# Kernel optimization log

Hardware: AMD Instinct MI355X
Metric: run time of the kernel (lower is better)

Reference implementation:

```python
import jax, jax.numpy as jnp
import numpy as np

C = 128       # in_channels
B = 256       # number of graph pairs (inter.shape[0])
N1_PER = 32   # nodes per graph, side 1
N2_PER = 32   # nodes per graph, side 2


def prelu(x, s):
    return jnp.where(x >= 0, x, s * x)


def _lin(k, fan_in, fan_out):
    return jax.random.normal(k, (fan_in, fan_out), jnp.float32) / np.sqrt(fan_in)


def setup_inputs() -> dict:
    key = jax.random.key(0)
    ks = jax.random.split(key, 16)
    N1, N2 = B * N1_PER, B * N2_PER
    d1 = np.full(B, N1_PER, np.int64)
    d2 = np.full(B, N2_PER, np.int64)
    batch_1 = np.repeat(np.arange(B), d1)
    batch_2 = np.repeat(np.arange(B), d2)
    # node offsets per graph (exclusive cumsum)
    s1 = np.concatenate([[0], np.cumsum(d1)[:-1]])
    s2 = np.concatenate([[0], np.cumsum(d2)[:-1]])
    # ragged pairwise cross-product indices, same as the torch loop
    ind_1 = np.concatenate([np.repeat(np.arange(d1[g]), d2[g]) + s1[g] for g in range(B)])
    ind_2 = np.concatenate([np.tile(np.arange(d2[g]), d1[g]) + s1[g] * 0 + s2[g] for g in range(B)])
    batch_ans = np.repeat(np.arange(B), d1 * d2)

    inp = {
        "x_1": jax.random.normal(ks[0], (N1, C), jnp.float32),
        "x_2": jax.random.normal(ks[1], (N2, C), jnp.float32),
        "inter": jax.random.normal(ks[2], (B, C), jnp.float32),
        "batch_1": jnp.asarray(batch_1, jnp.int32),
        "batch_2": jnp.asarray(batch_2, jnp.int32),
        "ind_1": jnp.asarray(ind_1, jnp.int32),
        "ind_2": jnp.asarray(ind_2, jnp.int32),
        "batch_ans": jnp.asarray(batch_ans, jnp.int32),
        # glorot-style param 'a'
        "a": jax.random.normal(ks[3], (C,), jnp.float32) * np.sqrt(2.0 / (1 + C)),
        # mlp: PReLU, Linear(2C,2C), PReLU, Linear(2C,C), PReLU, Linear(C,C)
        "Wm1": _lin(ks[4], 2 * C, 2 * C), "bm1": jnp.zeros((2 * C,), jnp.float32),
        "Wm2": _lin(ks[5], 2 * C, C),     "bm2": jnp.zeros((C,), jnp.float32),
        "Wm3": _lin(ks[6], C, C),         "bm3": jnp.zeros((C,), jnp.float32),
        "pm0": jnp.float32(0.25), "pm1": jnp.float32(0.25), "pm2": jnp.float32(0.25),
        # weight_1: Linear(2C,C), PReLU, Linear(C,1), Sigmoid
        "Wg1a": _lin(ks[7], 2 * C, C), "bg1a": jnp.zeros((C,), jnp.float32),
        "Wg1b": _lin(ks[8], C, 1),     "bg1b": jnp.zeros((1,), jnp.float32),
        "pw1": jnp.float32(0.25),
        # weight_2: Linear(2C,C), PReLU, Linear(C,1), Sigmoid
        "Wg2a": _lin(ks[9], 2 * C, C), "bg2a": jnp.zeros((C,), jnp.float32),
        "Wg2b": _lin(ks[10], C, 1),    "bg2b": jnp.zeros((1,), jnp.float32),
        "pw2": jnp.float32(0.25),
    }
    return inp


def reference(x_1, x_2, inter, batch_1, batch_2, ind_1, ind_2, batch_ans,
              a, Wm1, bm1, Wm2, bm2, Wm3, bm3, pm0, pm1, pm2,
              Wg1a, bg1a, Wg1b, bg1b, pw1, Wg2a, bg2a, Wg2b, bg2b, pw2):
    Bn = inter.shape[0]
    # global_add_pool readouts, broadcast back per node (repeat_interleave == gather by batch id)
    r1 = jax.ops.segment_sum(x_1, batch_1, num_segments=Bn)          # [B, C]
    r2 = jax.ops.segment_sum(x_2, batch_2, num_segments=Bn)          # [B, C]
    x1s = jnp.concatenate([x_1, r2[batch_1]], axis=1)                # [N1, 2C]
    x2s = jnp.concatenate([x_2, r1[batch_2]], axis=1)                # [N2, 2C]
    # gating MLPs -> sigmoid scalar per node
    w1 = jax.nn.sigmoid(prelu(x1s @ Wg1a + bg1a, pw1) @ Wg1b + bg1b)  # [N1, 1]
    w2 = jax.nn.sigmoid(prelu(x2s @ Wg2a + bg2a, pw2) @ Wg2b + bg2b)  # [N2, 1]
    x1g = x_1 * w1
    x2g = x_2 * w2
    # ragged pairwise gather
    xi = x1g[ind_1]                                                  # [P, C]
    xj = x2g[ind_2]                                                  # [P, C]
    h = jnp.concatenate([xi, xj], axis=1)                            # [P, 2C]
    h = prelu(h, pm0) @ Wm1 + bm1
    h = prelu(h, pm1) @ Wm2 + bm2
    h = prelu(h, pm2) @ Wm3 + bm3                                    # [P, C]
    ssi = (a * h) * inter[batch_ans]                                 # [P, C]
    logit = jax.ops.segment_sum(jnp.sum(ssi, axis=-1), batch_ans, num_segments=Bn)  # [B]
    return (logit, xi, xj)
```

## Files before the change

kernel.cpp:

```cpp
#include <hip/hip_runtime.h>
#include <hip/hip_bf16.h>
#include <hip/hip_fp16.h>

typedef __attribute__((ext_vector_type(8))) _Float16 half8;
typedef __attribute__((ext_vector_type(2))) _Float16 f16x2;
typedef __attribute__((ext_vector_type(8))) short short8;
typedef __attribute__((ext_vector_type(4))) float f32x4;

#define C_ 128

__device__ __forceinline__ unsigned short f2h(float f) {
    return __builtin_bit_cast(unsigned short, (_Float16)f);
}
__device__ __forceinline__ f16x2 pkrtz(float x, float y) {
    return __builtin_bit_cast(f16x2, __builtin_amdgcn_cvt_pkrtz(x, y));
}
__device__ __forceinline__ float prelu_f(float x, float s) {
    return fmaxf(x, 0.f) + s * fminf(x, 0.f);
}
__device__ __forceinline__ half8 prelu_h8(half8 x, half8 sl) {
    half8 z = {0, 0, 0, 0, 0, 0, 0, 0};
    half8 mx = __builtin_elementwise_max(x, z);
    half8 mn = __builtin_elementwise_min(x, z);
    return mn * sl + mx;
}

__global__ __launch_bounds__(256) void prep_weights(
    const float* __restrict__ Wm1, const float* __restrict__ Wm2,
    const float* __restrict__ Wg1a, const float* __restrict__ Wg2a,
    short* __restrict__ ws)
{
    int id = blockIdx.x * 256 + threadIdx.x;
    if (id < 8192) {
        int c = id >> 5, kb = (id & 31) * 8;
        short8 v;
        #pragma unroll
        for (int e = 0; e < 8; ++e) v[e] = (short)f2h(Wm1[(kb + e) * 256 + c]);
        *(short8*)(ws + c * 256 + kb) = v;
    }
    if (id < 4096) {
        int c = id >> 5, kb = (id & 31) * 8;
        short8 a, b, d;
        #pragma unroll
        for (int e = 0; e < 8; ++e) {
            a[e] = (short)f2h(Wm2 [(kb + e) * C_ + c]);
            b[e] = (short)f2h(Wg1a[(kb + e) * C_ + c]);
            d[e] = (short)f2h(Wg2a[(kb + e) * C_ + c]);
        }
        *(short8*)(ws + 65536  + c * 256 + kb) = a;
        *(short8*)(ws + 98304  + c * 256 + kb) = b;
        *(short8*)(ws + 131072 + c * 256 + kb) = d;
    }
}

__global__ __launch_bounds__(512, 1) void interactions_fused(
    const float* __restrict__ x1_, const float* __restrict__ x2_,
    const float* __restrict__ inter, const float* __restrict__ aP,
    const short* __restrict__ Wt,
    const float* __restrict__ bm1, const float* __restrict__ bm2,
    const float* __restrict__ Wm3, const float* __restrict__ bm3,
    const float* __restrict__ pm0p, const float* __restrict__ pm1p,
    const float* __restrict__ pm2p,
    const float* __restrict__ bg1a, const float* __restrict__ Wg1b,
    const float* __restrict__ bg1b, const float* __restrict__ pw1p,
    const float* __restrict__ bg2a, const float* __restrict__ Wg2b,
    const float* __restrict__ bg2b, const float* __restrict__ pw2p,
    float* __restrict__ out)
{
    __shared__ __align__(16) float xs1[32 * 132];
    __shared__ __align__(16) float xs2[32 * 132];
    __shared__ __align__(16) unsigned char Ub[16384];
    __shared__ __align__(16) unsigned char Vb[16384];
    __shared__ __align__(16) float rr[2][C_];
    __shared__ __align__(16) float tv[C_];
    __shared__ __align__(16) float ugs[C_];
    __shared__ float wgtp[2][2][32];
    __shared__ float red[4];
    __shared__ float cbias_s;
    __shared__ int cnt1, cnt2;

    const int t = threadIdx.x;
    const int g = blockIdx.x;
    const int lane = t & 63;
    const int w = t >> 6;

    if (t == 0) { cnt1 = 0; cnt2 = 0; }

    {
        const float* s1 = x1_ + (size_t)g * 4096;
        const float* s2 = x2_ + (size_t)g * 4096;
        #pragma unroll
        for (int q = 0; q < 2; ++q) {
            int idx = q * 512 + t;
            int row = idx >> 5, cc = (idx & 31) * 4;
            f32x4 v1 = *(const f32x4*)(s1 + idx * 4);
            f32x4 v2 = *(const f32x4*)(s2 + idx * 4);
            *(f32x4*)(xs1 + row * 132 + cc) = v1;
            *(f32x4*)(xs2 + row * 132 + cc) = v2;
        }
    }
    __syncthreads();

    if (t < 128) {
        float s = 0.f;
        for (int n = 0; n < 32; ++n) s += xs1[n * 132 + t];
        rr[0][t] = s;
    } else if (t < 256) {
        int c = t - 128;
        float s = 0.f;
        for (int n = 0; n < 32; ++n) s += xs2[n * 132 + c];
        rr[1][c] = s;
    } else if (t < 384) {
        int c = t - 256;
        tv[c] = aP[c] * inter[(size_t)g * C_ + c];
    }
    __syncthreads();

    {
        const int task = w & 3;
        const int half = w >> 2;
        const int sd = task >> 1;
        const int rt = task & 1;
        const float* xs = sd ? xs2 : xs1;
        const float* roth = sd ? rr[0] : rr[1];
        const short* WgT = Wt + (sd ? 131072 : 98304);
        const float* bga = sd ? bg2a : bg1a;
        const float* wgb = sd ? Wg2b : Wg1b;
        const float pw  = sd ? pw2p[0] : pw1p[0];
        const int row = rt * 16 + (lane & 15);
        const int kg = (lane >> 4) * 8;

        half8 afr[8];
        #pragma unroll
        for (int kt = 0; kt < 8; ++kt) {
            const float* p = (kt < 4) ? (xs + row * 132 + kt * 32 + kg)
                                      : (roth + (kt - 4) * 32 + kg);
            f32x4 lo = *(const f32x4*)p;
            f32x4 hi = *(const f32x4*)(p + 4);
            f16x2 a = pkrtz(lo[0], lo[1]);
            f16x2 b = pkrtz(lo[2], lo[3]);
            f16x2 c = pkrtz(hi[0], hi[1]);
            f16x2 d = pkrtz(hi[2], hi[3]);
            half8 fr = {a[0], a[1], b[0], b[1], c[0], c[1], d[0], d[1]};
            afr[kt] = fr;
        }
        float pr[4] = {0, 0, 0, 0};
        #pragma unroll
        for (int cq = 0; cq < 4; ++cq) {
            const int ct = half * 4 + cq;
            const int c = ct * 16 + (lane & 15);
            const short* wp = WgT + c * 256 + kg;
            f32x4 acc = {0, 0, 0, 0};
            #pragma unroll
            for (int kt = 0; kt < 8; ++kt)
                acc = __builtin_amdgcn_mfma_f32_16x16x32_f16(
                          afr[kt], *(const half8*)(wp + kt * 32), acc, 0, 0, 0);
            const float bgac = bga[c], wgbc = wgb[c];
            #pragma unroll
            for (int r = 0; r < 4; ++r)
                pr[r] += prelu_f(acc[r] + bgac, pw) * wgbc;
        }
        #pragma unroll
        for (int r = 0; r < 4; ++r) {
            float p = pr[r];
            p += __shfl_xor(p, 1); p += __shfl_xor(p, 2);
            p += __shfl_xor(p, 4); p += __shfl_xor(p, 8);
            if ((lane & 15) == 0)
                wgtp[half][sd][rt * 16 + (lane >> 4) * 4 + r] = p;
        }
    }
    __syncthreads();

    {
        const float bgb1 = bg1b[0], bgb2 = bg2b[0];
        const int cc = (t & 31) * 4;
        const int tn = t >> 5;
        #pragma unroll
        for (int m = 0; m < 2; ++m) {
            const int nr = m * 16 + tn;
            const float w1v = 1.f / (1.f + __expf(-(wgtp[0][0][nr] + wgtp[1][0][nr] + bgb1)));
            const float w2v = 1.f / (1.f + __expf(-(wgtp[0][1][nr] + wgtp[1][1][nr] + bgb2)));
            f32x4 v1 = *(f32x4*)(xs1 + nr * 132 + cc);
            f32x4 v2 = *(f32x4*)(xs2 + nr * 132 + cc);
            v1 *= w1v; v2 *= w2v;
            *(f32x4*)(xs1 + nr * 132 + cc) = v1;
            *(f32x4*)(xs2 + nr * 132 + cc) = v2;
        }
    }
    __syncthreads();

    if (w >= 4) {
        if (t < 384) {
            const int c = t - 256;
            const float* wr = Wm3 + c * C_;
            float s0 = 0, s1 = 0, s2 = 0, s3 = 0;
            #pragma unroll
            for (int k = 0; k < 128; k += 4) {
                f32x4 wv = *(const f32x4*)(wr + k);
                s0 += wv[0] * tv[k];     s1 += wv[1] * tv[k + 1];
                s2 += wv[2] * tv[k + 2]; s3 += wv[3] * tv[k + 3];
            }
            ugs[c] = (s0 + s1) + (s2 + s3);
        } else if (w == 7) {
            float p = bm3[lane] * tv[lane] + bm3[64 + lane] * tv[64 + lane];
            #pragma unroll
            for (int m = 1; m < 64; m <<= 1) p += __shfl_xor(p, m);
            if (lane == 0) cbias_s = p;
        }
        __threadfence_block();
        if (lane == 0)
            __hip_atomic_fetch_add(&cnt1, 1, __ATOMIC_RELEASE, __HIP_MEMORY_SCOPE_WORKGROUP);

        const int ws_ = w - 4;
        float* oxi = out + 256 + (size_t)g * 131072;
        float* oxj = out + 256 + 33554432 + (size_t)g * 131072;
        const int ccl = (lane & 31) * 4;

        #pragma unroll
        for (int blk = 0; blk < 8; ++blk) {
            const int i = ws_ * 8 + blk;
            f32x4 v = *(const f32x4*)(xs1 + i * 132 + ccl);
            float* base = oxi + i * 4096 + lane * 4;
            #pragma unroll
            for (int s2 = 0; s2 < 16; ++s2)
                __builtin_nontemporal_store(v, (f32x4*)(base + s2 * 256));
        }
        f32x4 vj[16];
        #pragma unroll
        for (int s2 = 0; s2 < 16; ++s2) {
            const int jn = (2 * s2 + (lane >> 5)) & 31;
            vj[s2] = *(const f32x4*)(xs2 + jn * 132 + ccl);
        }
        #pragma unroll
        for (int so = 0; so < 8; ++so) {
            float* bb = oxj + (size_t)(ws_ * 256 + so * 32) * 128 + lane * 4;
            #pragma unroll
            for (int s2 = 0; s2 < 16; ++s2)
                __builtin_nontemporal_store(vj[s2], (f32x4*)(bb + s2 * 256));
        }
    } else {
        {
            const int sd = w >> 1;
            const int rt = w & 1;
            const float* xs = sd ? xs2 : xs1;
            const float pm0 = pm0p[0];
            const int row = rt * 16 + (lane & 15);
            const int kg = (lane >> 4) * 8;
            half8 afr[4];
            #pragma unroll
            for (int kt = 0; kt < 4; ++kt) {
                const float* p = xs + row * 132 + kt * 32 + kg;
                f32x4 lo = *(const f32x4*)p;
                f32x4 hi = *(const f32x4*)(p + 4);
                f16x2 a = pkrtz(prelu_f(lo[0], pm0), prelu_f(lo[1], pm0));
                f16x2 b = pkrtz(prelu_f(lo[2], pm0), prelu_f(lo[3], pm0));
                f16x2 c = pkrtz(prelu_f(hi[0], pm0), prelu_f(hi[1], pm0));
                f16x2 d = pkrtz(prelu_f(hi[2], pm0), prelu_f(hi[3], pm0));
                half8 fr = {a[0], a[1], b[0], b[1], c[0], c[1], d[0], d[1]};
                afr[kt] = fr;
            }
            unsigned char* dst = sd ? Vb : Ub;
            #pragma unroll
            for (int ct = 0; ct < 16; ++ct) {
                const int c = ct * 16 + (lane & 15);
                const short* wp = Wt + c * 256 + sd * 128 + kg;
                f32x4 av = {0, 0, 0, 0};
                #pragma unroll
                for (int kt = 0; kt < 4; ++kt)
                    av = __builtin_amdgcn_mfma_f32_16x16x32_f16(
                             afr[kt], *(const half8*)(wp + kt * 32), av, 0, 0, 0);
                const float badd = sd ? 0.f : bm1[c];
                #pragma unroll
                for (int r = 0; r < 4; ++r) {
                    const int n = rt * 16 + (lane >> 4) * 4 + r;
                    const int off = n * 512 + ((2 * c + ((n & 7) << 6)) & 511);
                    *(unsigned short*)(dst + off) = f2h(av[r] + badd);
                }
            }
        }
        __threadfence_block();
        if (lane == 0)
            __hip_atomic_fetch_add(&cnt1, 1, __ATOMIC_RELEASE, __HIP_MEMORY_SCOPE_WORKGROUP);
        while (__hip_atomic_load(&cnt1, __ATOMIC_ACQUIRE, __HIP_MEMORY_SCOPE_WORKGROUP) < 8)
            __builtin_amdgcn_s_sleep(1);
        __threadfence_block();

        float psum = 0.f;
        {
            const float pm1v = pm1p[0], pm2v = pm2p[0];
            const _Float16 pm1s = (_Float16)pm1v;
            const half8 pm1h = {pm1s, pm1s, pm1s, pm1s, pm1s, pm1s, pm1s, pm1s};
            const int cl = lane & 15;
            const int kg8 = (lane >> 4) * 8;
            const int kg16 = kg8 * 2;
            const int c0 = (2 * w) * 16 + cl, c1 = (2 * w + 1) * 16 + cl;
            half8 Bf0[8], Bf1[8];
            const short* w2p0 = Wt + 65536 + c0 * 256 + kg8;
            const short* w2p1 = Wt + 65536 + c1 * 256 + kg8;
            #pragma unroll
            for (int kt = 0; kt < 8; ++kt) {
                Bf0[kt] = *(const half8*)(w2p0 + kt * 32);
                Bf1[kt] = *(const half8*)(w2p1 + kt * 32);
            }
            const float bm2c0 = bm2[c0], bm2c1 = bm2[c1];
            const float ug0 = ugs[c0], ug1 = ugs[c1];

            half8 VrA[8], VrB[8];
            {
                const int j0 = cl, j1 = 16 + cl;
                #pragma unroll
                for (int kt = 0; kt < 8; ++kt) {
                    const int koff = kt * 64 + kg16;
                    VrA[kt] = *(const half8*)(Vb + j0 * 512 + ((koff + ((j0 & 7) << 6)) & 511));
                    VrB[kt] = *(const half8*)(Vb + j1 * 512 + ((koff + ((j1 & 7) << 6)) & 511));
                }
            }

            #pragma unroll 2
            for (int i = 0; i < 32; ++i) {
                const int ub = i * 512, us = (i & 7) << 6;
                half8 u8[8];
                #pragma unroll
                for (int kt = 0; kt < 8; ++kt)
                    u8[kt] = *(const half8*)(Ub + ub + ((kt * 64 + kg16 + us) & 511));
                f32x4 acc0 = {0, 0, 0, 0}, acc1 = {0, 0, 0, 0};
                f32x4 acc2 = {0, 0, 0, 0}, acc3 = {0, 0, 0, 0};
                #pragma unroll
                for (int kt = 0; kt < 8; ++kt) {
                    half8 afA = prelu_h8(u8[kt] + VrA[kt], pm1h);
                    half8 afB = prelu_h8(u8[kt] + VrB[kt], pm1h);
                    acc0 = __builtin_amdgcn_mfma_f32_16x16x32_f16(afA, Bf0[kt], acc0, 0, 0, 0);
                    acc1 = __builtin_amdgcn_mfma_f32_16x16x32_f16(afA, Bf1[kt], acc1, 0, 0, 0);
                    acc2 = __builtin_amdgcn_mfma_f32_16x16x32_f16(afB, Bf0[kt], acc2, 0, 0, 0);
                    acc3 = __builtin_amdgcn_mfma_f32_16x16x32_f16(afB, Bf1[kt], acc3, 0, 0, 0);
                }
                #pragma unroll
                for (int r = 0; r < 4; ++r) {
                    psum += prelu_f(acc0[r] + bm2c0, pm2v) * ug0;
                    psum += prelu_f(acc1[r] + bm2c1, pm2v) * ug1;
                    psum += prelu_f(acc2[r] + bm2c0, pm2v) * ug0;
                    psum += prelu_f(acc3[r] + bm2c1, pm2v) * ug1;
                }
            }
        }
        #pragma unroll
        for (int m = 1; m < 64; m <<= 1) psum += __shfl_xor(psum, m);
        if (lane == 0) {
            red[w] = psum;
            __threadfence_block();
            __hip_atomic_fetch_add(&cnt2, 1, __ATOMIC_RELEASE, __HIP_MEMORY_SCOPE_WORKGROUP);
            if (w == 0) {
                while (__hip_atomic_load(&cnt2, __ATOMIC_ACQUIRE, __HIP_MEMORY_SCOPE_WORKGROUP) < 4)
                    __builtin_amdgcn_s_sleep(1);
                __threadfence_block();
                out[g] = red[0] + red[1] + red[2] + red[3] + 1024.f * cbias_s;
            }
        }
    }
}

extern "C" void kernel_launch(void* const* d_in, const int* in_sizes, int n_in,
                              void* d_out, int out_size, void* d_ws, size_t ws_size,
                              hipStream_t stream) {
    const float* x1   = (const float*)d_in[0];
    const float* x2   = (const float*)d_in[1];
    const float* itr  = (const float*)d_in[2];
    const float* a    = (const float*)d_in[8];
    const float* Wm1  = (const float*)d_in[9];
    const float* bm1  = (const float*)d_in[10];
    const float* Wm2  = (const float*)d_in[11];
    const float* bm2  = (const float*)d_in[12];
    const float* Wm3  = (const float*)d_in[13];
    const float* bm3  = (const float*)d_in[14];
    const float* pm0  = (const float*)d_in[15];
    const float* pm1  = (const float*)d_in[16];
    const float* pm2  = (const float*)d_in[17];
    const float* Wg1a = (const float*)d_in[18];
    const float* bg1a = (const float*)d_in[19];
    const float* Wg1b = (const float*)d_in[20];
    const float* bg1b = (const float*)d_in[21];
    const float* pw1  = (const float*)d_in[22];
    const float* Wg2a = (const float*)d_in[23];
    const float* bg2a = (const float*)d_in[24];
    const float* Wg2b = (const float*)d_in[25];
    const float* bg2b = (const float*)d_in[26];
    const float* pw2  = (const float*)d_in[27];
    float* out = (float*)d_out;
    short* Wt = (short*)d_ws;

    hipLaunchKernelGGL(prep_weights, dim3(32), dim3(256), 0, stream,
                       Wm1, Wm2, Wg1a, Wg2a, Wt);
    hipLaunchKernelGGL(interactions_fused, dim3(256), dim3(512), 0, stream,
                       x1, x2, itr, a, Wt, bm1, bm2, Wm3, bm3,
                       pm0, pm1, pm2, bg1a, Wg1b, bg1b, pw1,
                       bg2a, Wg2b, bg2b, pw2, out);
}
```

Before: 86.34 us.

## Distribute xi/xj output writes across all waves via shared work counter

```diff
diff --git a/kernel.cpp b/kernel.cpp
--- a/kernel.cpp
+++ b/kernel.cpp
@@ -77,14 +77,14 @@
     __shared__ float wgtp[2][2][32];
     __shared__ float red[4];
     __shared__ float cbias_s;
-    __shared__ int cnt1, cnt2;
+    __shared__ int cnt1, cnt2, ucnt;
 
     const int t = threadIdx.x;
     const int g = blockIdx.x;
     const int lane = t & 63;
     const int w = t >> 6;
 
-    if (t == 0) { cnt1 = 0; cnt2 = 0; }
+    if (t == 0) { cnt1 = 0; cnt2 = 0; ucnt = 0; }
 
     {
         const float* s1 = x1_ + (size_t)g * 4096;
@@ -210,34 +210,6 @@
         __threadfence_block();
         if (lane == 0)
             __hip_atomic_fetch_add(&cnt1, 1, __ATOMIC_RELEASE, __HIP_MEMORY_SCOPE_WORKGROUP);
-
-        const int ws_ = w - 4;
-        float* oxi = out + 256 + (size_t)g * 131072;
-        float* oxj = out + 256 + 33554432 + (size_t)g * 131072;
-        const int ccl = (lane & 31) * 4;
-
-        #pragma unroll
-        for (int blk = 0; blk < 8; ++blk) {
-            const int i = ws_ * 8 + blk;
-            f32x4 v = *(const f32x4*)(xs1 + i * 132 + ccl);
-            float* base = oxi + i * 4096 + lane * 4;
-            #pragma unroll
-            for (int s2 = 0; s2 < 16; ++s2)
-                __builtin_nontemporal_store(v, (f32x4*)(base + s2 * 256));
-        }
-        f32x4 vj[16];
-        #pragma unroll
-        for (int s2 = 0; s2 < 16; ++s2) {
-            const int jn = (2 * s2 + (lane >> 5)) & 31;
-            vj[s2] = *(const f32x4*)(xs2 + jn * 132 + ccl);
-        }
-        #pragma unroll
-        for (int so = 0; so < 8; ++so) {
-            float* bb = oxj + (size_t)(ws_ * 256 + so * 32) * 128 + lane * 4;
-            #pragma unroll
-            for (int s2 = 0; s2 < 16; ++s2)
-                __builtin_nontemporal_store(vj[s2], (f32x4*)(bb + s2 * 256));
-        }
     } else {
         {
             const int sd = w >> 1;
@@ -354,6 +326,40 @@
                     __builtin_amdgcn_s_sleep(1);
                 __threadfence_block();
                 out[g] = red[0] + red[1] + red[2] + red[3] + 1024.f * cbias_s;
+            }
+        }
+    }
+
+    {
+        float* oxi = out + 256 + (size_t)g * 131072;
+        float* oxj = out + 256 + 33554432 + (size_t)g * 131072;
+        const int ccl = (lane & 31) * 4;
+
+        f32x4 vj[16];
+        #pragma unroll
+        for (int s2 = 0; s2 < 16; ++s2) {
+            const int jn = 2 * s2 + (lane >> 5);
+            vj[s2] = *(const f32x4*)(xs2 + jn * 132 + ccl);
+        }
+
+        for (;;) {
+            int u = 0;
+            if (lane == 0)
+                u = __hip_atomic_fetch_add(&ucnt, 1, __ATOMIC_RELAXED,
+                                           __HIP_MEMORY_SCOPE_WORKGROUP);
+            u = __shfl(u, 0);
+            if (u >= 64) break;
+            if (u < 32) {
+                f32x4 v = *(const f32x4*)(xs1 + u * 132 + ccl);
+                float* base = oxi + u * 4096 + lane * 4;
+                #pragma unroll
+                for (int s2 = 0; s2 < 16; ++s2)
+                    *(f32x4*)(base + s2 * 256) = v;
+            } else {
+                float* bb = oxj + (size_t)(u - 32) * 4096 + lane * 4;
+                #pragma unroll
+                for (int s2 = 0; s2 < 16; ++s2)
+                    *(f32x4*)(bb + s2 * 256) = vj[s2];
             }
         }
     }
```

Result: faster. 83.70 us (-3.0%).

## Split fused kernel into compute stage and wide expand/logit kernel

Applied to the files above, without the earlier changes.

```diff
diff --git a/kernel.cpp b/kernel.cpp
--- a/kernel.cpp
+++ b/kernel.cpp
@@ -8,6 +8,7 @@
 typedef __attribute__((ext_vector_type(4))) float f32x4;
 
 #define C_ 128
+#define XJ_OFF 33554432
 
 __device__ __forceinline__ unsigned short f2h(float f) {
     return __builtin_bit_cast(unsigned short, (_Float16)f);
@@ -53,50 +54,37 @@
     }
 }
 
-__global__ __launch_bounds__(512, 1) void interactions_fused(
+__global__ __launch_bounds__(256, 2) void compute_stage(
     const float* __restrict__ x1_, const float* __restrict__ x2_,
     const float* __restrict__ inter, const float* __restrict__ aP,
     const short* __restrict__ Wt,
-    const float* __restrict__ bm1, const float* __restrict__ bm2,
     const float* __restrict__ Wm3, const float* __restrict__ bm3,
-    const float* __restrict__ pm0p, const float* __restrict__ pm1p,
-    const float* __restrict__ pm2p,
     const float* __restrict__ bg1a, const float* __restrict__ Wg1b,
     const float* __restrict__ bg1b, const float* __restrict__ pw1p,
     const float* __restrict__ bg2a, const float* __restrict__ Wg2b,
     const float* __restrict__ bg2b, const float* __restrict__ pw2p,
-    float* __restrict__ out)
+    float* __restrict__ wsF, float* __restrict__ out)
 {
     __shared__ __align__(16) float xs1[32 * 132];
     __shared__ __align__(16) float xs2[32 * 132];
-    __shared__ __align__(16) unsigned char Ub[16384];
-    __shared__ __align__(16) unsigned char Vb[16384];
     __shared__ __align__(16) float rr[2][C_];
     __shared__ __align__(16) float tv[C_];
-    __shared__ __align__(16) float ugs[C_];
-    __shared__ float wgtp[2][2][32];
-    __shared__ float red[4];
-    __shared__ float cbias_s;
-    __shared__ int cnt1, cnt2;
+    __shared__ float wgt[2][32];
 
     const int t = threadIdx.x;
     const int g = blockIdx.x;
     const int lane = t & 63;
     const int w = t >> 6;
 
-    if (t == 0) { cnt1 = 0; cnt2 = 0; }
-
     {
         const float* s1 = x1_ + (size_t)g * 4096;
         const float* s2 = x2_ + (size_t)g * 4096;
         #pragma unroll
-        for (int q = 0; q < 2; ++q) {
-            int idx = q * 512 + t;
+        for (int q = 0; q < 4; ++q) {
+            int idx = q * 256 + t;
             int row = idx >> 5, cc = (idx & 31) * 4;
-            f32x4 v1 = *(const f32x4*)(s1 + idx * 4);
-            f32x4 v2 = *(const f32x4*)(s2 + idx * 4);
-            *(f32x4*)(xs1 + row * 132 + cc) = v1;
-            *(f32x4*)(xs2 + row * 132 + cc) = v2;
+            *(f32x4*)(xs1 + row * 132 + cc) = *(const f32x4*)(s1 + idx * 4);
+            *(f32x4*)(xs2 + row * 132 + cc) = *(const f32x4*)(s2 + idx * 4);
         }
     }
     __syncthreads();
@@ -105,27 +93,24 @@
         float s = 0.f;
         for (int n = 0; n < 32; ++n) s += xs1[n * 132 + t];
         rr[0][t] = s;
-    } else if (t < 256) {
+        tv[t] = aP[t] * inter[(size_t)g * C_ + t];
+    } else {
         int c = t - 128;
         float s = 0.f;
         for (int n = 0; n < 32; ++n) s += xs2[n * 132 + c];
         rr[1][c] = s;
-    } else if (t < 384) {
-        int c = t - 256;
-        tv[c] = aP[c] * inter[(size_t)g * C_ + c];
-    }
-    __syncthreads();
-
-    {
-        const int task = w & 3;
-        const int half = w >> 2;
-        const int sd = task >> 1;
-        const int rt = task & 1;
+    }
+    __syncthreads();
+
+    {
+        const int sd = w >> 1;
+        const int rt = w & 1;
         const float* xs = sd ? xs2 : xs1;
         const float* roth = sd ? rr[0] : rr[1];
         const short* WgT = Wt + (sd ? 131072 : 98304);
         const float* bga = sd ? bg2a : bg1a;
         const float* wgb = sd ? Wg2b : Wg1b;
+        const float bgb = sd ? bg2b[0] : bg1b[0];
         const float pw  = sd ? pw2p[0] : pw1p[0];
         const int row = rt * 16 + (lane & 15);
         const int kg = (lane >> 4) * 8;
@@ -146,8 +131,7 @@
         }
         float pr[4] = {0, 0, 0, 0};
         #pragma unroll
-        for (int cq = 0; cq < 4; ++cq) {
-            const int ct = half * 4 + cq;
+        for (int ct = 0; ct < 8; ++ct) {
             const int c = ct * 16 + (lane & 15);
             const short* wp = WgT + c * 256 + kg;
             f32x4 acc = {0, 0, 0, 0};
@@ -166,20 +150,19 @@
             p += __shfl_xor(p, 1); p += __shfl_xor(p, 2);
             p += __shfl_xor(p, 4); p += __shfl_xor(p, 8);
             if ((lane & 15) == 0)
-                wgtp[half][sd][rt * 16 + (lane >> 4) * 4 + r] = p;
-        }
-    }
-    __syncthreads();
-
-    {
-        const float bgb1 = bg1b[0], bgb2 = bg2b[0];
+                wgt[sd][rt * 16 + (lane >> 4) * 4 + r] =
+                    1.f / (1.f + __expf(-(p + bgb)));
+        }
+    }
+    __syncthreads();
+
+    {
         const int cc = (t & 31) * 4;
         const int tn = t >> 5;
         #pragma unroll
-        for (int m = 0; m < 2; ++m) {
-            const int nr = m * 16 + tn;
-            const float w1v = 1.f / (1.f + __expf(-(wgtp[0][0][nr] + wgtp[1][0][nr] + bgb1)));
-            const float w2v = 1.f / (1.f + __expf(-(wgtp[0][1][nr] + wgtp[1][1][nr] + bgb2)));
+        for (int m = 0; m < 4; ++m) {
+            const int nr = m * 8 + tn;
+            const float w1v = wgt[0][nr], w2v = wgt[1][nr];
             f32x4 v1 = *(f32x4*)(xs1 + nr * 132 + cc);
             f32x4 v2 = *(f32x4*)(xs2 + nr * 132 + cc);
             v1 *= w1v; v2 *= w2v;
@@ -189,10 +172,20 @@
     }
     __syncthreads();
 
-    if (w >= 4) {
-        if (t < 384) {
-            const int c = t - 256;
-            const float* wr = Wm3 + c * C_;
+    {
+        float* oxi = out + 256 + (size_t)g * 131072;
+        float* oxj = oxi + XJ_OFF;
+        #pragma unroll
+        for (int m = 0; m < 4; ++m) {
+            const int row = m * 8 + (t >> 5);
+            const int c4 = (t & 31) * 4;
+            *(f32x4*)(oxi + row * 4096 + c4) = *(const f32x4*)(xs1 + row * 132 + c4);
+            const int idx4 = m * 256 + t;
+            const int j = idx4 >> 5;
+            *(f32x4*)(oxj + idx4 * 4) = *(const f32x4*)(xs2 + j * 132 + (idx4 & 31) * 4);
+        }
+        if (t < 128) {
+            const float* wr = Wm3 + t * C_;
             float s0 = 0, s1 = 0, s2 = 0, s3 = 0;
             #pragma unroll
             for (int k = 0; k < 128; k += 4) {
@@ -200,163 +193,180 @@
                 s0 += wv[0] * tv[k];     s1 += wv[1] * tv[k + 1];
                 s2 += wv[2] * tv[k + 2]; s3 += wv[3] * tv[k + 3];
             }
-            ugs[c] = (s0 + s1) + (s2 + s3);
-        } else if (w == 7) {
+            wsF[g * 132 + t] = (s0 + s1) + (s2 + s3);
+        } else if (t < 192) {
             float p = bm3[lane] * tv[lane] + bm3[64 + lane] * tv[64 + lane];
             #pragma unroll
             for (int m = 1; m < 64; m <<= 1) p += __shfl_xor(p, m);
-            if (lane == 0) cbias_s = p;
-        }
-        __threadfence_block();
-        if (lane == 0)
-            __hip_atomic_fetch_add(&cnt1, 1, __ATOMIC_RELEASE, __HIP_MEMORY_SCOPE_WORKGROUP);
-
-        const int ws_ = w - 4;
-        float* oxi = out + 256 + (size_t)g * 131072;
-        float* oxj = out + 256 + 33554432 + (size_t)g * 131072;
-        const int ccl = (lane & 31) * 4;
-
-        #pragma unroll
-        for (int blk = 0; blk < 8; ++blk) {
-            const int i = ws_ * 8 + blk;
-            f32x4 v = *(const f32x4*)(xs1 + i * 132 + ccl);
-            float* base = oxi + i * 4096 + lane * 4;
-            #pragma unroll
-            for (int s2 = 0; s2 < 16; ++s2)
-                __builtin_nontemporal_store(v, (f32x4*)(base + s2 * 256));
-        }
-        f32x4 vj[16];
-        #pragma unroll
-        for (int s2 = 0; s2 < 16; ++s2) {
-            const int jn = (2 * s2 + (lane >> 5)) & 31;
-            vj[s2] = *(const f32x4*)(xs2 + jn * 132 + ccl);
-        }
-        #pragma unroll
-        for (int so = 0; so < 8; ++so) {
-            float* bb = oxj + (size_t)(ws_ * 256 + so * 32) * 128 + lane * 4;
-            #pragma unroll
-            for (int s2 = 0; s2 < 16; ++s2)
-                __builtin_nontemporal_store(vj[s2], (f32x4*)(bb + s2 * 256));
-        }
-    } else {
+            if (lane == 0) wsF[g * 132 + 128] = p;
+        }
+    }
+}
+
+__global__ __launch_bounds__(256) void expand_logit(
+    const short* __restrict__ Wt, const float* __restrict__ wsF,
+    const float* __restrict__ bm1, const float* __restrict__ bm2,
+    const float* __restrict__ pm0p, const float* __restrict__ pm1p,
+    const float* __restrict__ pm2p, float* __restrict__ out)
+{
+    const int b = blockIdx.x;
+    const int t = threadIdx.x;
+
+    if (b >= 256) {
+        const int sb = b - 256;
+        for (int u = sb; u < 16384; u += 1792) {
+            const int g = u >> 6, r = u & 63;
+            float* oxi = out + 256 + (size_t)g * 131072;
+            if (r < 32) {
+                const f32x4 v = *(const f32x4*)(oxi + r * 4096 + (t & 31) * 4);
+                float* base = oxi + r * 4096;
+                #pragma unroll
+                for (int s = 0; s < 4; ++s)
+                    *(f32x4*)(base + (s * 256 + t) * 4) = v;
+            } else {
+                float* oxj = oxi + XJ_OFF;
+                const int i = r - 32;
+                #pragma unroll
+                for (int s = 0; s < 4; ++s) {
+                    const int idx4 = s * 256 + t;
+                    f32x4 v = *(const f32x4*)(oxj + idx4 * 4);
+                    *(f32x4*)(oxj + i * 4096 + idx4 * 4) = v;
+                }
+            }
+        }
+        return;
+    }
+
+    __shared__ __align__(16) float xs1[32 * 132];
+    __shared__ __align__(16) float xs2[32 * 132];
+    __shared__ __align__(16) unsigned char Ub[16384];
+    __shared__ __align__(16) unsigned char Vb[16384];
+    __shared__ __align__(16) float ugs[C_];
+    __shared__ float red[4];
+
+    const int g = b;
+    const int lane = t & 63;
+    const int w = t >> 6;
+    const float* oxi = out + 256 + (size_t)g * 131072;
+    const float* oxj = oxi + XJ_OFF;
+
+    #pragma unroll
+    for (int m = 0; m < 4; ++m) {
+        const int row = m * 8 + (t >> 5);
+        const int c4 = (t & 31) * 4;
+        *(f32x4*)(xs1 + row * 132 + c4) = *(const f32x4*)(oxi + row * 4096 + c4);
+        const int idx4 = m * 256 + t;
+        const int j = idx4 >> 5;
+        *(f32x4*)(xs2 + j * 132 + (idx4 & 31) * 4) = *(const f32x4*)(oxj + idx4 * 4);
+    }
+    if (t < 128) ugs[t] = wsF[g * 132 + t];
+    __syncthreads();
+
+    {
+        const int sd = w >> 1;
+        const int rt = w & 1;
+        const float* xs = sd ? xs2 : xs1;
+        const float pm0 = pm0p[0];
+        const int row = rt * 16 + (lane & 15);
+        const int kg = (lane >> 4) * 8;
+        half8 afr[4];
+        #pragma unroll
+        for (int kt = 0; kt < 4; ++kt) {
+            const float* p = xs + row * 132 + kt * 32 + kg;
+            f32x4 lo = *(const f32x4*)p;
+            f32x4 hi = *(const f32x4*)(p + 4);
+            f16x2 a = pkrtz(prelu_f(lo[0], pm0), prelu_f(lo[1], pm0));
+            f16x2 b = pkrtz(prelu_f(lo[2], pm0), prelu_f(lo[3], pm0));
+            f16x2 c = pkrtz(prelu_f(hi[0], pm0), prelu_f(hi[1], pm0));
+            f16x2 d = pkrtz(prelu_f(hi[2], pm0), prelu_f(hi[3], pm0));
+            half8 fr = {a[0], a[1], b[0], b[1], c[0], c[1], d[0], d[1]};
+            afr[kt] = fr;
+        }
+        unsigned char* dst = sd ? Vb : Ub;
+        #pragma unroll
+        for (int ct = 0; ct < 16; ++ct) {
+            const int c = ct * 16 + (lane & 15);
+            const short* wp = Wt + c * 256 + sd * 128 + kg;
+            f32x4 av = {0, 0, 0, 0};
+            #pragma unroll
+            for (int kt = 0; kt < 4; ++kt)
+                av = __builtin_amdgcn_mfma_f32_16x16x32_f16(
+                         afr[kt], *(const half8*)(wp + kt * 32), av, 0, 0, 0);
+            const float badd = sd ? 0.f : bm1[c];
+            #pragma unroll
+            for (int r = 0; r < 4; ++r) {
+                const int n = rt * 16 + (lane >> 4) * 4 + r;
+                const int off = n * 512 + ((2 * c + ((n & 7) << 6)) & 511);
+                *(unsigned short*)(dst + off) = f2h(av[r] + badd);
+            }
+        }
+    }
+    __syncthreads();
+
+    float psum = 0.f;
+    {
+        const float pm1v = pm1p[0], pm2v = pm2p[0];
+        const _Float16 pm1s = (_Float16)pm1v;
+        const half8 pm1h = {pm1s, pm1s, pm1s, pm1s, pm1s, pm1s, pm1s, pm1s};
+        const int cl = lane & 15;
+        const int kg8 = (lane >> 4) * 8;
+        const int kg16 = kg8 * 2;
+        const int c0 = (2 * w) * 16 + cl, c1 = (2 * w + 1) * 16 + cl;
+        half8 Bf0[8], Bf1[8];
+        const short* w2p0 = Wt + 65536 + c0 * 256 + kg8;
+        const short* w2p1 = Wt + 65536 + c1 * 256 + kg8;
+        #pragma unroll
+        for (int kt = 0; kt < 8; ++kt) {
+            Bf0[kt] = *(const half8*)(w2p0 + kt * 32);
+            Bf1[kt] = *(const half8*)(w2p1 + kt * 32);
+        }
+        const float bm2c0 = bm2[c0], bm2c1 = bm2[c1];
+        const float ug0 = ugs[c0], ug1 = ugs[c1];
+
+        half8 VrA[8], VrB[8];
         {
-            const int sd = w >> 1;
-            const int rt = w & 1;
-            const float* xs = sd ? xs2 : xs1;
-            const float pm0 = pm0p[0];
-            const int row = rt * 16 + (lane & 15);
-            const int kg = (lane >> 4) * 8;
-            half8 afr[4];
-            #pragma unroll
-            for (int kt = 0; kt < 4; ++kt) {
-                const float* p = xs + row * 132 + kt * 32 + kg;
-                f32x4 lo = *(const f32x4*)p;
-                f32x4 hi = *(const f32x4*)(p + 4);
-                f16x2 a = pkrtz(prelu_f(lo[0], pm0), prelu_f(lo[1], pm0));
-                f16x2 b = pkrtz(prelu_f(lo[2], pm0), prelu_f(lo[3], pm0));
-                f16x2 c = pkrtz(prelu_f(hi[0], pm0), prelu_f(hi[1], pm0));
-                f16x2 d = pkrtz(prelu_f(hi[2], pm0), prelu_f(hi[3], pm0));
-                half8 fr = {a[0], a[1], b[0], b[1], c[0], c[1], d[0], d[1]};
-                afr[kt] = fr;
-            }
-            unsigned char* dst = sd ? Vb : Ub;
-            #pragma unroll
-            for (int ct = 0; ct < 16; ++ct) {
-                const int c = ct * 16 + (lane & 15);
-                const short* wp = Wt + c * 256 + sd * 128 + kg;
-                f32x4 av = {0, 0, 0, 0};
-                #pragma unroll
-                for (int kt = 0; kt < 4; ++kt)
-                    av = __builtin_amdgcn_mfma_f32_16x16x32_f16(
-                             afr[kt], *(const half8*)(wp + kt * 32), av, 0, 0, 0);
-                const float badd = sd ? 0.f : bm1[c];
-                #pragma unroll
-                for (int r = 0; r < 4; ++r) {
-                    const int n = rt * 16 + (lane >> 4) * 4 + r;
-                    const int off = n * 512 + ((2 * c + ((n & 7) << 6)) & 511);
-                    *(unsigned short*)(dst + off) = f2h(av[r] + badd);
-                }
-            }
-        }
-        __threadfence_block();
-        if (lane == 0)
-            __hip_atomic_fetch_add(&cnt1, 1, __ATOMIC_RELEASE, __HIP_MEMORY_SCOPE_WORKGROUP);
-        while (__hip_atomic_load(&cnt1, __ATOMIC_ACQUIRE, __HIP_MEMORY_SCOPE_WORKGROUP) < 8)
-            __builtin_amdgcn_s_sleep(1);
-        __threadfence_block();
-
-        float psum = 0.f;
-        {
-            const float pm1v = pm1p[0], pm2v = pm2p[0];
-            const _Float16 pm1s = (_Float16)pm1v;
-            const half8 pm1h = {pm1s, pm1s, pm1s, pm1s, pm1s, pm1s, pm1s, pm1s};
-            const int cl = lane & 15;
-            const int kg8 = (lane >> 4) * 8;
-            const int kg16 = kg8 * 2;
-            const int c0 = (2 * w) * 16 + cl, c1 = (2 * w + 1) * 16 + cl;
-            half8 Bf0[8], Bf1[8];
-            const short* w2p0 = Wt + 65536 + c0 * 256 + kg8;
-            const short* w2p1 = Wt + 65536 + c1 * 256 + kg8;
+            const int j0 = cl, j1 = 16 + cl;
             #pragma unroll
             for (int kt = 0; kt < 8; ++kt) {
-                Bf0[kt] = *(const half8*)(w2p0 + kt * 32);
-                Bf1[kt] = *(const half8*)(w2p1 + kt * 32);
-            }
-            const float bm2c0 = bm2[c0], bm2c1 = bm2[c1];
-            const float ug0 = ugs[c0], ug1 = ugs[c1];
-
-            half8 VrA[8], VrB[8];
-            {
-                const int j0 = cl, j1 = 16 + cl;
-                #pragma unroll
-                for (int kt = 0; kt < 8; ++kt) {
-                    const int koff = kt * 64 + kg16;
-                    VrA[kt] = *(const half8*)(Vb + j0 * 512 + ((koff + ((j0 & 7) << 6)) & 511));
-                    VrB[kt] = *(const half8*)(Vb + j1 * 512 + ((koff + ((j1 & 7) << 6)) & 511));
-                }
-            }
-
-            #pragma unroll 2
-            for (int i = 0; i < 32; ++i) {
-                const int ub = i * 512, us = (i & 7) << 6;
-                half8 u8[8];
-                #pragma unroll
-                for (int kt = 0; kt < 8; ++kt)
-                    u8[kt] = *(const half8*)(Ub + ub + ((kt * 64 + kg16 + us) & 511));
-                f32x4 acc0 = {0, 0, 0, 0}, acc1 = {0, 0, 0, 0};
-                f32x4 acc2 = {0, 0, 0, 0}, acc3 = {0, 0, 0, 0};
-                #pragma unroll
-                for (int kt = 0; kt < 8; ++kt) {
-                    half8 afA = prelu_h8(u8[kt] + VrA[kt], pm1h);
-                    half8 afB = prelu_h8(u8[kt] + VrB[kt], pm1h);
-                    acc0 = __builtin_amdgcn_mfma_f32_16x16x32_f16(afA, Bf0[kt], acc0, 0, 0, 0);
-                    acc1 = __builtin_amdgcn_mfma_f32_16x16x32_f16(afA, Bf1[kt], acc1, 0, 0, 0);
-                    acc2 = __builtin_amdgcn_mfma_f32_16x16x32_f16(afB, Bf0[kt], acc2, 0, 0, 0);
-                    acc3 = __builtin_amdgcn_mfma_f32_16x16x32_f16(afB, Bf1[kt], acc3, 0, 0, 0);
-                }
-                #pragma unroll
-                for (int r = 0; r < 4; ++r) {
-                    psum += prelu_f(acc0[r] + bm2c0, pm2v) * ug0;
-                    psum += prelu_f(acc1[r] + bm2c1, pm2v) * ug1;
-                    psum += prelu_f(acc2[r] + bm2c0, pm2v) * ug0;
-                    psum += prelu_f(acc3[r] + bm2c1, pm2v) * ug1;
-                }
-            }
-        }
-        #pragma unroll
-        for (int m = 1; m < 64; m <<= 1) psum += __shfl_xor(psum, m);
-        if (lane == 0) {
-            red[w] = psum;
-            __threadfence_block();
-            __hip_atomic_fetch_add(&cnt2, 1, __ATOMIC_RELEASE, __HIP_MEMORY_SCOPE_WORKGROUP);
-            if (w == 0) {
-                while (__hip_atomic_load(&cnt2, __ATOMIC_ACQUIRE, __HIP_MEMORY_SCOPE_WORKGROUP) < 4)
-                    __builtin_amdgcn_s_sleep(1);
-                __threadfence_block();
-                out[g] = red[0] + red[1] + red[2] + red[3] + 1024.f * cbias_s;
-            }
-        }
-    }
+                const int koff = kt * 64 + kg16;
+                VrA[kt] = *(const half8*)(Vb + j0 * 512 + ((koff + ((j0 & 7) << 6)) & 511));
+                VrB[kt] = *(const half8*)(Vb + j1 * 512 + ((koff + ((j1 & 7) << 6)) & 511));
+            }
+        }
+
+        #pragma unroll 2
+        for (int i = 0; i < 32; ++i) {
+            const int ub = i * 512, us = (i & 7) << 6;
+            half8 u8[8];
+            #pragma unroll
+            for (int kt = 0; kt < 8; ++kt)
+                u8[kt] = *(const half8*)(Ub + ub + ((kt * 64 + kg16 + us) & 511));
+            f32x4 acc0 = {0, 0, 0, 0}, acc1 = {0, 0, 0, 0};
+            f32x4 acc2 = {0, 0, 0, 0}, acc3 = {0, 0, 0, 0};
+            #pragma unroll
+            for (int kt = 0; kt < 8; ++kt) {
+                half8 afA = prelu_h8(u8[kt] + VrA[kt], pm1h);
+                half8 afB = prelu_h8(u8[kt] + VrB[kt], pm1h);
+                acc0 = __builtin_amdgcn_mfma_f32_16x16x32_f16(afA, Bf0[kt], acc0, 0, 0, 0);
+                acc1 = __builtin_amdgcn_mfma_f32_16x16x32_f16(afA, Bf1[kt], acc1, 0, 0, 0);
+                acc2 = __builtin_amdgcn_mfma_f32_16x16x32_f16(afB, Bf0[kt], acc2, 0, 0, 0);
+                acc3 = __builtin_amdgcn_mfma_f32_16x16x32_f16(afB, Bf1[kt], acc3, 0, 0, 0);
+            }
+            #pragma unroll
+            for (int r = 0; r < 4; ++r) {
+                psum += prelu_f(acc0[r] + bm2c0, pm2v) * ug0;
+                psum += prelu_f(acc1[r] + bm2c1, pm2v) * ug1;
+                psum += prelu_f(acc2[r] + bm2c0, pm2v) * ug0;
+                psum += prelu_f(acc3[r] + bm2c1, pm2v) * ug1;
+            }
+        }
+    }
+    #pragma unroll
+    for (int m = 1; m < 64; m <<= 1) psum += __shfl_xor(psum, m);
+    if (lane == 0) red[w] = psum;
+    __syncthreads();
+    if (t == 0)
+        out[g] = red[0] + red[1] + red[2] + red[3] + 1024.f * wsF[g * 132 + 128];
 }
 
 extern "C" void kernel_launch(void* const* d_in, const int* in_sizes, int n_in,
@@ -387,11 +397,14 @@
     const float* pw2  = (const float*)d_in[27];
     float* out = (float*)d_out;
     short* Wt = (short*)d_ws;
+    float* wsF = (float*)(Wt + 163840);
 
     hipLaunchKernelGGL(prep_weights, dim3(32), dim3(256), 0, stream,
                        Wm1, Wm2, Wg1a, Wg2a, Wt);
-    hipLaunchKernelGGL(interactions_fused, dim3(256), dim3(512), 0, stream,
-                       x1, x2, itr, a, Wt, bm1, bm2, Wm3, bm3,
-                       pm0, pm1, pm2, bg1a, Wg1b, bg1b, pw1,
-                       bg2a, Wg2b, bg2b, pw2, out);
-}
+    hipLaunchKernelGGL(compute_stage, dim3(256), dim3(256), 0, stream,
+                       x1, x2, itr, a, Wt, Wm3, bm3,
+                       bg1a, Wg1b, bg1b, pw1, bg2a, Wg2b, bg2b, pw2,
+                       wsF, out);
+    hipLaunchKernelGGL(expand_logit, dim3(2048), dim3(256), 0, stream,
+                       Wt, wsF, bm1, bm2, pm0, pm1, pm2, out);
+}
```

Result: slower. 93.98 us (+8.9%).

## Split xi/xj output broadcast into a separate wide expansion kernel

Applied to the files above, without the earlier changes.

```diff
diff --git a/kernel.cpp b/kernel.cpp
--- a/kernel.cpp
+++ b/kernel.cpp
@@ -8,6 +8,7 @@
 typedef __attribute__((ext_vector_type(4))) float f32x4;
 
 #define C_ 128
+#define XJ_OFF 33554432
 
 __device__ __forceinline__ unsigned short f2h(float f) {
     return __builtin_bit_cast(unsigned short, (_Float16)f);
@@ -53,7 +54,7 @@
     }
 }
 
-__global__ __launch_bounds__(512, 1) void interactions_fused(
+__global__ __launch_bounds__(512, 1) void interactions_core(
     const float* __restrict__ x1_, const float* __restrict__ x2_,
     const float* __restrict__ inter, const float* __restrict__ aP,
     const short* __restrict__ Wt,
@@ -93,10 +94,8 @@
         for (int q = 0; q < 2; ++q) {
             int idx = q * 512 + t;
             int row = idx >> 5, cc = (idx & 31) * 4;
-            f32x4 v1 = *(const f32x4*)(s1 + idx * 4);
-            f32x4 v2 = *(const f32x4*)(s2 + idx * 4);
-            *(f32x4*)(xs1 + row * 132 + cc) = v1;
-            *(f32x4*)(xs2 + row * 132 + cc) = v2;
+            *(f32x4*)(xs1 + row * 132 + cc) = *(const f32x4*)(s1 + idx * 4);
+            *(f32x4*)(xs2 + row * 132 + cc) = *(const f32x4*)(s2 + idx * 4);
         }
     }
     __syncthreads();
@@ -189,6 +188,9 @@
     }
     __syncthreads();
 
+    float* oxi = out + 256 + (size_t)g * 131072;
+    float* oxj = oxi + XJ_OFF;
+
     if (w >= 4) {
         if (t < 384) {
             const int c = t - 256;
@@ -211,32 +213,24 @@
         if (lane == 0)
             __hip_atomic_fetch_add(&cnt1, 1, __ATOMIC_RELEASE, __HIP_MEMORY_SCOPE_WORKGROUP);
 
-        const int ws_ = w - 4;
-        float* oxi = out + 256 + (size_t)g * 131072;
-        float* oxj = out + 256 + 33554432 + (size_t)g * 131072;
-        const int ccl = (lane & 31) * 4;
-
-        #pragma unroll
-        for (int blk = 0; blk < 8; ++blk) {
-            const int i = ws_ * 8 + blk;
-            f32x4 v = *(const f32x4*)(xs1 + i * 132 + ccl);
-            float* base = oxi + i * 4096 + lane * 4;
-            #pragma unroll
-            for (int s2 = 0; s2 < 16; ++s2)
-                __builtin_nontemporal_store(v, (f32x4*)(base + s2 * 256));
-        }
-        f32x4 vj[16];
-        #pragma unroll
-        for (int s2 = 0; s2 < 16; ++s2) {
-            const int jn = (2 * s2 + (lane >> 5)) & 31;
-            vj[s2] = *(const f32x4*)(xs2 + jn * 132 + ccl);
-        }
-        #pragma unroll
-        for (int so = 0; so < 8; ++so) {
-            float* bb = oxj + (size_t)(ws_ * 256 + so * 32) * 128 + lane * 4;
-            #pragma unroll
-            for (int s2 = 0; s2 < 16; ++s2)
-                __builtin_nontemporal_store(vj[s2], (f32x4*)(bb + s2 * 256));
+        if (w < 6) {
+            const int base = (w - 4) * 512;
+            #pragma unroll
+            for (int m = 0; m < 8; ++m) {
+                const int idx = base + m * 64 + lane;
+                const int row = idx >> 5, c4 = (idx & 31) * 4;
+                *(f32x4*)(oxi + (size_t)row * 4096 + c4) =
+                    *(const f32x4*)(xs1 + row * 132 + c4);
+            }
+        } else {
+            const int base = (w - 6) * 512;
+            #pragma unroll
+            for (int m = 0; m < 8; ++m) {
+                const int idx = base + m * 64 + lane;
+                const int row = idx >> 5, c4 = (idx & 31) * 4;
+                *(f32x4*)(oxj + idx * 4) =
+                    *(const f32x4*)(xs2 + row * 132 + c4);
+            }
         }
     } else {
         {
@@ -355,6 +349,40 @@
                 __threadfence_block();
                 out[g] = red[0] + red[1] + red[2] + red[3] + 1024.f * cbias_s;
             }
+        }
+    }
+}
+
+__global__ __launch_bounds__(256) void expand_out(float* __restrict__ out)
+{
+    const int b = blockIdx.x;
+    const int t = threadIdx.x;
+
+    if (b < 256) {
+        float* oxi = out + 256 + (size_t)b * 131072;
+        const int c4 = (t & 31) * 4;
+        f32x4 v[32];
+        #pragma unroll
+        for (int i = 0; i < 32; ++i)
+            v[i] = *(const f32x4*)(oxi + (size_t)i * 4096 + c4);
+        #pragma unroll
+        for (int i = 0; i < 32; ++i) {
+            float* base = oxi + (size_t)i * 4096;
+            #pragma unroll
+            for (int s = 0; s < 4; ++s)
+                *(f32x4*)(base + (s * 256 + t) * 4) = v[i];
+        }
+    } else {
+        float* oxj = out + 256 + XJ_OFF + (size_t)(b - 256) * 131072;
+        f32x4 vj[4];
+        #pragma unroll
+        for (int s = 0; s < 4; ++s)
+            vj[s] = *(const f32x4*)(oxj + (s * 256 + t) * 4);
+        for (int i = 1; i < 32; ++i) {
+            float* base = oxj + (size_t)i * 4096;
+            #pragma unroll
+            for (int s = 0; s < 4; ++s)
+                *(f32x4*)(base + (s * 256 + t) * 4) = vj[s];
         }
     }
 }
@@ -390,8 +418,9 @@
 
     hipLaunchKernelGGL(prep_weights, dim3(32), dim3(256), 0, stream,
                        Wm1, Wm2, Wg1a, Wg2a, Wt);
-    hipLaunchKernelGGL(interactions_fused, dim3(256), dim3(512), 0, stream,
+    hipLaunchKernelGGL(interactions_core, dim3(256), dim3(512), 0, stream,
                        x1, x2, itr, a, Wt, bm1, bm2, Wm3, bm3,
                        pm0, pm1, pm2, bg1a, Wg1b, bg1b, pw1,
                        bg2a, Wg2b, bg2b, pw2, out);
-}
+    hipLaunchKernelGGL(expand_out, dim3(512), dim3(256), 0, stream, out);
+}
```

Measured after the change: 110.5 us. 28.0% more time.
